# Kernel tuning notes

Hardware: AMD Instinct MI355X
Metric: run time of the kernel (lower is better)

## Reference

```python
import jax, jax.numpy as jnp
import numpy as np

N, E, H, ED, S = 20000, 320000, 256, 64, 4  # nodes, edges, hidden, edge_dim, message_steps


def setup_inputs() -> dict:
    key = jax.random.key(0)
    ks = jax.random.split(key, 20)
    w = lambda k, shape: jax.random.normal(k, shape, dtype=jnp.float32) * 0.02
    inp = {
        "node_state": jax.random.normal(ks[0], (N, H), dtype=jnp.float32),
        "edge_attr": jax.random.normal(ks[1], (E, ED), dtype=jnp.float32),
        # per-step stacked parameters (S steps)
        "nn_g": jnp.ones((S, H), jnp.float32),  # node_norm gamma
        "nn_b": jnp.zeros((S, H), jnp.float32),
        "mn_g": jnp.ones((S, H), jnp.float32),  # msg_norm gamma
        "mn_b": jnp.zeros((S, H), jnp.float32),
        "eW1": w(ks[2], (S, 2 * H + ED, H)), "eb1": jnp.zeros((S, H), jnp.float32),
        "eW2": w(ks[3], (S, H, H)),          "eb2": jnp.zeros((S, H), jnp.float32),
        "nW1": w(ks[4], (S, 2 * H, 2 * H)),  "nb1": jnp.zeros((S, 2 * H), jnp.float32),
        "nW2": w(ks[5], (S, 2 * H, H)),      "nb2": jnp.zeros((S, H), jnp.float32),
        "edge_index": jax.random.randint(ks[6], (2, E), 0, N, dtype=jnp.int64),
    }
    return inp


def _layer_norm(x, g, b, eps=1e-5):
    m = jnp.mean(x, axis=-1, keepdims=True)
    v = jnp.var(x, axis=-1, keepdims=True)
    return (x - m) * jax.lax.rsqrt(v + eps) * g + b


def reference(node_state, edge_attr, nn_g, nn_b, mn_g, mn_b,
              eW1, eb1, eW2, eb2, nW1, nb1, nW2, nb2, edge_index):
    n = node_state.shape[0]
    src, dst = edge_index[0], edge_index[1]
    ones = jnp.ones((dst.shape[0], 1), node_state.dtype)
    deg = jax.ops.segment_sum(ones, dst, num_segments=n)  # [N,1], same each step
    deg = jnp.maximum(deg, 1.0)
    h = node_state
    for i in range(nn_g.shape[0]):  # fixed small number of message steps
        hn = _layer_norm(h, nn_g[i], nn_b[i])                       # [N,H]
        x = jnp.concatenate([hn[src], hn[dst], edge_attr], axis=1)  # [E,2H+ED]
        msg = jax.nn.silu(x @ eW1[i] + eb1[i]) @ eW2[i] + eb2[i]    # [E,H]
        agg = jax.ops.segment_sum(msg, dst, num_segments=n)         # [N,H]
        agg = _layer_norm(agg / deg, mn_g[i], mn_b[i])
        y = jnp.concatenate([hn, agg], axis=1)                      # [N,2H]
        h = h + (jax.nn.silu(y @ nW1[i] + nb1[i]) @ nW2[i] + nb2[i])
    return h
```

## Files before the change

### kernel.cpp

```cpp
#include <hip/hip_runtime.h>
#include <hip/hip_bf16.h>
#include <stdint.h>

#define NN 20000
#define NE 320000
#define HH 256
#define EDK 64
#define NSTEPS 4
#define ECH 80000
#define NCHUNK 4
#define WSTEP 606208

typedef __attribute__((ext_vector_type(8))) short bf16x8;
typedef __attribute__((ext_vector_type(4))) float f32x4;

__device__ __forceinline__ float silu_f(float x) { return x / (1.0f + __expf(-x)); }

__device__ __forceinline__ unsigned short f2bf(float f) {
    __hip_bfloat16 h = __float2bfloat16(f);
    return __builtin_bit_cast(unsigned short, h);
}
__device__ __forceinline__ float bf2f(unsigned short u) {
    unsigned int x = ((unsigned int)u) << 16;
    return __builtin_bit_cast(float, x);
}
__device__ __forceinline__ unsigned int pk2(float a, float b) {
    return (unsigned int)f2bf(a) | ((unsigned int)f2bf(b) << 16);
}

__global__ void ln_kernel(const float* __restrict__ x, const float* __restrict__ g,
                          const float* __restrict__ b, float* __restrict__ y, int M)
{
    int row  = blockIdx.x * 4 + (threadIdx.x >> 6);
    int lane = threadIdx.x & 63;
    if (row >= M) return;
    float4 v = *(const float4*)(x + (size_t)row * HH + lane * 4);
    float s  = v.x + v.y + v.z + v.w;
    float ss = v.x*v.x + v.y*v.y + v.z*v.z + v.w*v.w;
#pragma unroll
    for (int off = 32; off > 0; off >>= 1) {
        s  += __shfl_down(s, off);
        ss += __shfl_down(ss, off);
    }
    float mean = __shfl(s, 0) * (1.0f / HH);
    float ms   = __shfl(ss, 0) * (1.0f / HH);
    float rstd = rsqrtf(ms - mean * mean + 1e-5f);
    float4 gg = *(const float4*)(g + lane * 4);
    float4 bb = *(const float4*)(b + lane * 4);
    float4 o;
    o.x = (v.x - mean) * rstd * gg.x + bb.x;
    o.y = (v.y - mean) * rstd * gg.y + bb.y;
    o.z = (v.z - mean) * rstd * gg.z + bb.z;
    o.w = (v.w - mean) * rstd * gg.w + bb.w;
    *(float4*)(y + (size_t)row * HH + lane * 4) = o;
}

__global__ void wtr_kernel(const float* __restrict__ eW1, const float* __restrict__ eW2,
                           const float* __restrict__ nW1, const float* __restrict__ nW2,
                           unsigned short* __restrict__ wbuf)
{
    int bx = blockIdx.x;
    int s  = bx / 592, t = bx % 592;
    const float* e1 = eW1 + (size_t)s * 576 * 256;
    unsigned short* wb = wbuf + (size_t)s * WSTEP;
    const float* src; unsigned short* dst; int K, N;
    if      (t < 64)  { src = e1;                          K = 256; N = 256; dst = wb; }
    else if (t < 128) { src = e1 + 65536;                  K = 256; N = 256; dst = wb + 65536;  t -= 64; }
    else if (t < 144) { src = e1 + 131072;                 K = 64;  N = 256; dst = wb + 131072; t -= 128; }
    else if (t < 208) { src = eW2 + (size_t)s * 65536;     K = 256; N = 256; dst = wb + 147456; t -= 144; }
    else if (t < 464) { src = nW1 + (size_t)s * 262144;    K = 512; N = 512; dst = wb + 212992; t -= 208; }
    else              { src = nW2 + (size_t)s * 131072;    K = 512; N = 256; dst = wb + 475136; t -= 464; }
    int ntn = N >> 5;
    int tk = t / ntn, tn = t % ntn;
    int k0 = tk * 32, n0 = tn * 32;
    __shared__ float ts[32][33];
    int tx = threadIdx.x & 31, ty = threadIdx.x >> 5;
#pragma unroll
    for (int i = 0; i < 4; i++)
        ts[ty + i * 8][tx] = src[(size_t)(k0 + ty + i * 8) * N + n0 + tx];
    __syncthreads();
#pragma unroll
    for (int i = 0; i < 4; i++)
        dst[(size_t)(n0 + ty + i * 8) * K + k0 + tx] = f2bf(ts[tx][ty + i * 8]);
}

__global__ void easort_kernel(const float* __restrict__ ea, const int* __restrict__ eorig,
                              unsigned short* __restrict__ out)
{
    int gid = blockIdx.x * 256 + threadIdx.x;
    int p = gid >> 4, q = gid & 15;
    if (p >= NE) return;
    float4 v = *(const float4*)(ea + (size_t)eorig[p] * EDK + q * 4);
    ushort4 o;
    o.x = f2bf(v.x); o.y = f2bf(v.y); o.z = f2bf(v.z); o.w = f2bf(v.w);
    *(ushort4*)(out + (size_t)p * EDK + q * 4) = o;
}

#define GBM 128
#define GBN 128
#define GBK 64
template <int EPI, int ASRC, bool BF16OUT>
__global__ __launch_bounds__(256) void mgemm(
    const void* __restrict__ A, const float* __restrict__ A2, int lda,
    const unsigned short* __restrict__ BT,
    const float* __restrict__ bias, const int* __restrict__ cnt,
    void* __restrict__ Cout, int M, int Nc, int K)
{
    __shared__ unsigned short smem[GBM * GBK + GBN * GBK];
    unsigned short* lsA = smem;
    unsigned short* lsB = smem + GBM * GBK;
    const int tid = threadIdx.x;
    const int row0 = blockIdx.x * GBM, col0 = blockIdx.y * GBN;
    const int r = tid >> 1, half = tid & 1;
    const int w = tid >> 6, l = tid & 63;
    const int wm = w >> 1, wn = w & 1;

    const float* Af = (const float*)A;
    const unsigned short* Ab = (const unsigned short*)A;
    int grow = row0 + r;
    bool aval = (grow < M);
    const unsigned short* brow = BT + (size_t)(col0 + r) * K;

    f32x4 acc[4][4] = {};

    for (int k0 = 0; k0 < K; k0 += GBK) {
        if constexpr (ASRC == 3) {
            uint4 q[4] = {};
            if (aval) {
                const unsigned short* ap = Ab + (size_t)grow * lda + k0 + half * 32;
#pragma unroll
                for (int ci = 0; ci < 4; ci++) q[ci] = ((const uint4*)ap)[ci];
            }
#pragma unroll
            for (int ci = 0; ci < 4; ci++) {
                int slot = half * 4 + ci;
                int phys = slot ^ (r & 7);
                *(uint4*)&lsA[r * GBK + phys * 8] = q[ci];
            }
        } else {
            const float* ap = nullptr;
            if constexpr (ASRC == 2) {
                if (aval) ap = ((k0 < 256) ? Af : A2) + (size_t)grow * 256 + (k0 & 255) + half * 32;
            } else {
                if (aval) ap = Af + (size_t)grow * lda + k0 + half * 32;
            }
            float4 fv[8];
            if (ap) {
#pragma unroll
                for (int i = 0; i < 8; i++) fv[i] = ((const float4*)ap)[i];
            } else {
#pragma unroll
                for (int i = 0; i < 8; i++) fv[i] = make_float4(0.f, 0.f, 0.f, 0.f);
            }
#pragma unroll
            for (int ci = 0; ci < 4; ci++) {
                uint4 q;
                q.x = pk2(fv[2*ci].x,   fv[2*ci].y);
                q.y = pk2(fv[2*ci].z,   fv[2*ci].w);
                q.z = pk2(fv[2*ci+1].x, fv[2*ci+1].y);
                q.w = pk2(fv[2*ci+1].z, fv[2*ci+1].w);
                int slot = half * 4 + ci;
                int phys = slot ^ (r & 7);
                *(uint4*)&lsA[r * GBK + phys * 8] = q;
            }
        }
        {
            const unsigned short* bp = brow + k0 + half * 32;
#pragma unroll
            for (int ci = 0; ci < 4; ci++) {
                uint4 q = ((const uint4*)bp)[ci];
                int slot = half * 4 + ci;
                int phys = slot ^ (r & 7);
                *(uint4*)&lsB[r * GBK + phys * 8] = q;
            }
        }
        __syncthreads();
#pragma unroll
        for (int ks = 0; ks < 2; ks++) {
            bf16x8 bfr[4];
#pragma unroll
            for (int n = 0; n < 4; n++) {
                int rn = wn * 64 + n * 16 + (l & 15);
                int phys = (ks * 4 + (l >> 4)) ^ (rn & 7);
                bfr[n] = *(bf16x8*)&lsB[rn * GBK + phys * 8];
            }
#pragma unroll
            for (int m = 0; m < 4; m++) {
                int rm = wm * 64 + m * 16 + (l & 15);
                int phys = (ks * 4 + (l >> 4)) ^ (rm & 7);
                bf16x8 af = *(bf16x8*)&lsA[rm * GBK + phys * 8];
#pragma unroll
                for (int n = 0; n < 4; n++)
                    acc[m][n] = __builtin_amdgcn_mfma_f32_16x16x32_bf16(af, bfr[n], acc[m][n], 0, 0, 0);
            }
        }
        __syncthreads();
    }

    if constexpr (BF16OUT) {
        unsigned short* Cb = (unsigned short*)Cout;
#pragma unroll
        for (int n = 0; n < 4; n++) {
            int cl = wn * 64 + n * 16 + (l & 15);
            float bv = bias ? bias[col0 + cl] : 0.0f;
#pragma unroll
            for (int m = 0; m < 4; m++) {
                int rbase = wm * 64 + m * 16 + (l >> 4) * 4;
#pragma unroll
                for (int i = 0; i < 4; i++) {
                    int rl = rbase + i;
                    float o = acc[m][n][i] + bv;
                    if (EPI == 1) o = silu_f(o);
                    int chunk = cl >> 3;
                    int phys = chunk ^ (rl & 15);
                    smem[rl * 128 + phys * 8 + (cl & 7)] = f2bf(o);
                }
            }
        }
        __syncthreads();
        int orow = tid >> 1, hf = tid & 1;
        int rr = row0 + orow;
        if (rr < M) {
            unsigned short* crow = Cb + (size_t)rr * Nc + col0;
#pragma unroll
            for (int c8 = 0; c8 < 8; c8++) {
                int chunk = hf * 8 + c8;
                int phys = chunk ^ (orow & 15);
                uint4 v = *(uint4*)&smem[orow * 128 + phys * 8];
                *(uint4*)(crow + chunk * 8) = v;
            }
        }
    } else {
        float* Cf = (float*)Cout;
        const int cbase = col0 + wn * 64 + (l & 15);
#pragma unroll
        for (int n = 0; n < 4; n++) {
            int c = cbase + n * 16;
            float bv = bias ? bias[c] : 0.0f;
#pragma unroll
            for (int m = 0; m < 4; m++) {
                int rbase = row0 + wm * 64 + m * 16 + (l >> 4) * 4;
#pragma unroll
                for (int i = 0; i < 4; i++) {
                    int rr = rbase + i;
                    if (rr >= M) continue;
                    float o = acc[m][n][i];
                    if (EPI == 2) {
                        float cf = (float)cnt[rr];
                        o = (o + cf * bv) / fmaxf(cf, 1.0f);
                    } else {
                        o += bv;
                        if (EPI == 1) o = silu_f(o);
                    }
                    size_t off = (size_t)rr * Nc + c;
                    if (EPI == 3) Cf[off] += o;
                    else          Cf[off] = o;
                }
            }
        }
    }
}

__global__ void agg_kernel(const unsigned short* __restrict__ Pab,
                           const unsigned short* __restrict__ Pe, const int* __restrict__ esrc,
                           const int* __restrict__ rowptr,
                           float* __restrict__ u, int e0, int e1)
{
    int node = blockIdx.x * 4 + (threadIdx.x >> 6);
    if (node >= NN) return;
    int beg = rowptr[node], end = rowptr[node + 1];
    int lo = beg > e0 ? beg : e0;
    int hi = end < e1 ? end : e1;
    if (lo >= hi) return;
    int lane = threadIdx.x & 63;
    int j = lane * 4;
    ushort4 pb4 = *(const ushort4*)(Pab + (size_t)node * 512 + 256 + j);
    float b0 = bf2f(pb4.x), b1 = bf2f(pb4.y), b2 = bf2f(pb4.z), b3 = bf2f(pb4.w);
    float a0 = 0.f, a1 = 0.f, a2 = 0.f, a3 = 0.f;
    int src_n = esrc[lo];
    for (int p = lo; p < hi; ++p) {
        int src = src_n;
        if (p + 1 < hi) src_n = esrc[p + 1];
        ushort4 pa4 = *(const ushort4*)(Pab + (size_t)src * 512 + j);
        ushort4 pe4 = *(const ushort4*)(Pe + (size_t)(p - e0) * HH + j);
        a0 += silu_f(bf2f(pa4.x) + b0 + bf2f(pe4.x));
        a1 += silu_f(bf2f(pa4.y) + b1 + bf2f(pe4.y));
        a2 += silu_f(bf2f(pa4.z) + b2 + bf2f(pe4.z));
        a3 += silu_f(bf2f(pa4.w) + b3 + bf2f(pe4.w));
    }
    float* up = u + (size_t)node * HH + j;
    float4 uo = *(const float4*)up;
    uo.x += a0; uo.y += a1; uo.z += a2; uo.w += a3;
    *(float4*)up = uo;
}

__global__ void detect_kernel(const uint32_t* __restrict__ w, int* flag)
{
    int i = blockIdx.x * 256 + threadIdx.x;
    bool bad = false;
    if (i < NE) {
        uint32_t lo = w[2 * i], hi = w[2 * i + 1];
        bad = (hi != 0u) || (lo >= (uint32_t)NN);
    }
    if (__any(bad)) {
        if ((threadIdx.x & 63) == 0) atomicAnd(flag, 0);
    }
}
__global__ void convert_kernel(const uint32_t* __restrict__ w, const int* __restrict__ flag,
                               int* __restrict__ out)
{
    int i = blockIdx.x * 256 + threadIdx.x;
    if (i >= 2 * NE) return;
    out[i] = (*flag) ? (int)w[2 * i] : (int)w[i];
}
__global__ void deg_kernel(const int* __restrict__ idx, int* __restrict__ cnt)
{
    int e = blockIdx.x * 256 + threadIdx.x;
    if (e < NE) atomicAdd(cnt + idx[NE + e], 1);
}

__global__ void scan_kernel(const int* __restrict__ cnt, int* __restrict__ rowptr)
{
    __shared__ int part[1024];
    const int T = 1024, PER = (NN + T - 1) / T;
    int t = threadIdx.x;
    int base = t * PER;
    int s = 0;
    for (int i = 0; i < PER; i++) {
        int idx = base + i;
        if (idx < NN) s += cnt[idx];
    }
    part[t] = s;
    __syncthreads();
    for (int off = 1; off < T; off <<= 1) {
        int v = (t >= off) ? part[t - off] : 0;
        __syncthreads();
        part[t] += v;
        __syncthreads();
    }
    int run = (t == 0) ? 0 : part[t - 1];
    for (int i = 0; i < PER; i++) {
        int idx = base + i;
        if (idx < NN) { rowptr[idx] = run; run += cnt[idx]; }
    }
    if (t == T - 1) rowptr[NN] = part[T - 1];
}

__global__ void fill_kernel(const int* __restrict__ idx, const int* __restrict__ rowptr,
                            int* __restrict__ fillc, int* __restrict__ esrc,
                            int* __restrict__ eorig)
{
    int e = blockIdx.x * 256 + threadIdx.x;
    if (e >= NE) return;
    int dst = idx[NE + e];
    int pos = rowptr[dst] + atomicAdd(fillc + dst, 1);
    esrc[pos]  = idx[e];
    eorig[pos] = e;
}

extern "C" void kernel_launch(void* const* d_in, const int* in_sizes, int n_in,
                              void* d_out, int out_size, void* d_ws, size_t ws_size,
                              hipStream_t stream)
{
    const float* node_state = (const float*)d_in[0];
    const float* edge_attr  = (const float*)d_in[1];
    const float* nn_g = (const float*)d_in[2];
    const float* nn_b = (const float*)d_in[3];
    const float* mn_g = (const float*)d_in[4];
    const float* mn_b = (const float*)d_in[5];
    const float* eW1  = (const float*)d_in[6];
    const float* eb1  = (const float*)d_in[7];
    const float* eW2  = (const float*)d_in[8];
    const float* eb2  = (const float*)d_in[9];
    const float* nW1  = (const float*)d_in[10];
    const float* nb1  = (const float*)d_in[11];
    const float* nW2  = (const float*)d_in[12];
    const float* nb2  = (const float*)d_in[13];
    const uint32_t* eidx_raw = (const uint32_t*)d_in[14];

    const size_t SZ = (size_t)NN * HH;
    float* hn = (float*)d_ws;
    float* u  = hn + SZ;
    unsigned short* Pab = (unsigned short*)(u + SZ);
    unsigned short* eas = Pab + (size_t)NN * 512;
    unsigned short* Pe  = eas + (size_t)NE * EDK;
    float* aggb = (float*)Pe;
    unsigned short* zb = (unsigned short*)((char*)Pe + (size_t)NN * HH * 4);
    unsigned short* wbuf = Pe + (size_t)ECH * HH;
    int* idx32  = (int*)(wbuf + 4 * WSTEP);
    int* esrc   = idx32 + 2 * NE;
    int* eorig  = esrc + NE;
    int* rowptr = eorig + NE;
    int* cnt    = rowptr + NN + 1;
    int* fillc  = cnt + NN;
    int* flag   = fillc + NN;
    size_t needed = ((size_t)(flag + 1) - (size_t)d_ws);
    if (ws_size < needed) return;

    float* h = (float*)d_out;

    hipMemcpyAsync(h, node_state, SZ * sizeof(float), hipMemcpyDeviceToDevice, stream);

    wtr_kernel<<<4 * 592, 256, 0, stream>>>(eW1, eW2, nW1, nW2, wbuf);
    hipMemsetAsync(flag, 0xFF, sizeof(int), stream);
    detect_kernel<<<(NE + 255) / 256, 256, 0, stream>>>(eidx_raw, flag);
    convert_kernel<<<(2 * NE + 255) / 256, 256, 0, stream>>>(eidx_raw, flag, idx32);
    hipMemsetAsync(cnt, 0, NN * sizeof(int), stream);
    deg_kernel<<<(NE + 255) / 256, 256, 0, stream>>>(idx32, cnt);
    scan_kernel<<<1, 1024, 0, stream>>>(cnt, rowptr);
    hipMemsetAsync(fillc, 0, NN * sizeof(int), stream);
    fill_kernel<<<(NE + 255) / 256, 256, 0, stream>>>(idx32, rowptr, fillc, esrc, eorig);
    easort_kernel<<<(NE * 16) / 256, 256, 0, stream>>>(edge_attr, eorig, eas);

    const dim3 gN2((NN + GBM - 1) / GBM, 2);
    const dim3 gN4((NN + GBM - 1) / GBM, 4);
    const dim3 gPe(ECH / GBM, 2);

    for (int s = 0; s < NSTEPS; s++) {
        const unsigned short* wb = wbuf + (size_t)s * WSTEP;
        const unsigned short* WabT = wb;
        const unsigned short* WcT  = wb + 131072;
        const unsigned short* eW2T = wb + 147456;
        const unsigned short* nW1T = wb + 212992;
        const unsigned short* nW2T = wb + 475136;
        const float* eb1s = eb1 + (size_t)s * HH;
        const float* eb2s = eb2 + (size_t)s * HH;
        const float* nb1s = nb1 + (size_t)s * 512;
        const float* nb2s = nb2 + (size_t)s * HH;

        ln_kernel<<<NN / 4, 256, 0, stream>>>(h, nn_g + s * HH, nn_b + s * HH, hn, NN);
        mgemm<0, 0, true><<<gN4, 256, 0, stream>>>(hn, nullptr, HH, WabT, nullptr, nullptr, Pab, NN, 512, HH);
        hipMemsetAsync(u, 0, SZ * sizeof(float), stream);
        for (int c = 0; c < NCHUNK; c++) {
            int e0 = c * ECH, e1 = e0 + ECH;
            mgemm<0, 3, true><<<gPe, 256, 0, stream>>>(eas + (size_t)e0 * EDK, nullptr, EDK, WcT, eb1s, nullptr, Pe, ECH, HH, EDK);
            agg_kernel<<<(NN + 3) / 4, 256, 0, stream>>>(Pab, Pe, esrc, rowptr, u, e0, e1);
        }
        mgemm<2, 0, false><<<gN2, 256, 0, stream>>>(u, nullptr, HH, eW2T, eb2s, cnt, aggb, NN, HH, HH);
        ln_kernel<<<NN / 4, 256, 0, stream>>>(aggb, mn_g + s * HH, mn_b + s * HH, aggb, NN);
        mgemm<1, 2, true><<<gN4, 256, 0, stream>>>(hn, aggb, HH, nW1T, nb1s, nullptr, zb, NN, 512, 512);
        mgemm<3, 3, false><<<gN2, 256, 0, stream>>>(zb, nullptr, 512, nW2T, nb2s, nullptr, h, NN, HH, 512);
    }
}
```

Before: 1.855 ms.

## Store intermediates in bf16, halve edge chunks, and prefetch in aggregation

LayerNorm outputs, the aggregation buffer and the message-norm output are now stored as bf16 rather than fp32. GEMMs read them directly as bf16 with no in-kernel conversion, which cuts memory traffic. Edge processing uses two chunks of 160000 instead of four. The first aggregation pass overwrites the buffer, so the memset is gone, and the gather loop is software-pipelined one edge ahead. The trade-off is accumulating partial sums in bf16 across chunks, which loses precision, and a larger Pe workspace that relies on hard-coded buffer offsets.

```diff
diff --git a/kernel.cpp b/kernel.cpp
--- a/kernel.cpp
+++ b/kernel.cpp
@@ -7,8 +7,8 @@
 #define HH 256
 #define EDK 64
 #define NSTEPS 4
-#define ECH 80000
-#define NCHUNK 4
+#define ECH 160000
+#define NCHUNK 2
 #define WSTEP 606208
 
 typedef __attribute__((ext_vector_type(8))) short bf16x8;
@@ -29,7 +29,7 @@
 }
 
 __global__ void ln_kernel(const float* __restrict__ x, const float* __restrict__ g,
-                          const float* __restrict__ b, float* __restrict__ y, int M)
+                          const float* __restrict__ b, unsigned short* __restrict__ y, int M)
 {
     int row  = blockIdx.x * 4 + (threadIdx.x >> 6);
     int lane = threadIdx.x & 63;
@@ -47,12 +47,12 @@
     float rstd = rsqrtf(ms - mean * mean + 1e-5f);
     float4 gg = *(const float4*)(g + lane * 4);
     float4 bb = *(const float4*)(b + lane * 4);
-    float4 o;
-    o.x = (v.x - mean) * rstd * gg.x + bb.x;
-    o.y = (v.y - mean) * rstd * gg.y + bb.y;
-    o.z = (v.z - mean) * rstd * gg.z + bb.z;
-    o.w = (v.w - mean) * rstd * gg.w + bb.w;
-    *(float4*)(y + (size_t)row * HH + lane * 4) = o;
+    ushort4 o;
+    o.x = f2bf((v.x - mean) * rstd * gg.x + bb.x);
+    o.y = f2bf((v.y - mean) * rstd * gg.y + bb.y);
+    o.z = f2bf((v.z - mean) * rstd * gg.z + bb.z);
+    o.w = f2bf((v.w - mean) * rstd * gg.w + bb.w);
+    *(ushort4*)(y + (size_t)row * HH + lane * 4) = o;
 }
 
 __global__ void wtr_kernel(const float* __restrict__ eW1, const float* __restrict__ eW2,
@@ -101,7 +101,7 @@
 #define GBK 64
 template <int EPI, int ASRC, bool BF16OUT>
 __global__ __launch_bounds__(256) void mgemm(
-    const void* __restrict__ A, const float* __restrict__ A2, int lda,
+    const void* __restrict__ A, const void* __restrict__ A2, int lda,
     const unsigned short* __restrict__ BT,
     const float* __restrict__ bias, const int* __restrict__ cnt,
     void* __restrict__ Cout, int M, int Nc, int K)
@@ -117,6 +117,7 @@
 
     const float* Af = (const float*)A;
     const unsigned short* Ab = (const unsigned short*)A;
+    const unsigned short* A2b = (const unsigned short*)A2;
     int grow = row0 + r;
     bool aval = (grow < M);
     const unsigned short* brow = BT + (size_t)(col0 + r) * K;
@@ -124,10 +125,14 @@
     f32x4 acc[4][4] = {};
 
     for (int k0 = 0; k0 < K; k0 += GBK) {
-        if constexpr (ASRC == 3) {
+        if constexpr (ASRC == 3 || ASRC == 4) {
             uint4 q[4] = {};
             if (aval) {
-                const unsigned short* ap = Ab + (size_t)grow * lda + k0 + half * 32;
+                const unsigned short* ap;
+                if constexpr (ASRC == 4)
+                    ap = ((k0 < 256) ? Ab : A2b) + (size_t)grow * 256 + (k0 & 255) + half * 32;
+                else
+                    ap = Ab + (size_t)grow * lda + k0 + half * 32;
 #pragma unroll
                 for (int ci = 0; ci < 4; ci++) q[ci] = ((const uint4*)ap)[ci];
             }
@@ -138,14 +143,9 @@
                 *(uint4*)&lsA[r * GBK + phys * 8] = q[ci];
             }
         } else {
-            const float* ap = nullptr;
-            if constexpr (ASRC == 2) {
-                if (aval) ap = ((k0 < 256) ? Af : A2) + (size_t)grow * 256 + (k0 & 255) + half * 32;
-            } else {
-                if (aval) ap = Af + (size_t)grow * lda + k0 + half * 32;
-            }
             float4 fv[8];
-            if (ap) {
+            if (aval) {
+                const float* ap = Af + (size_t)grow * lda + k0 + half * 32;
 #pragma unroll
                 for (int i = 0; i < 8; i++) fv[i] = ((const float4*)ap)[i];
             } else {
@@ -261,37 +261,52 @@
     }
 }
 
+template <bool FIRST>
 __global__ void agg_kernel(const unsigned short* __restrict__ Pab,
                            const unsigned short* __restrict__ Pe, const int* __restrict__ esrc,
                            const int* __restrict__ rowptr,
-                           float* __restrict__ u, int e0, int e1)
+                           unsigned short* __restrict__ u, int e0, int e1)
 {
     int node = blockIdx.x * 4 + (threadIdx.x >> 6);
     if (node >= NN) return;
     int beg = rowptr[node], end = rowptr[node + 1];
     int lo = beg > e0 ? beg : e0;
     int hi = end < e1 ? end : e1;
-    if (lo >= hi) return;
+    if (!FIRST && lo >= hi) return;
     int lane = threadIdx.x & 63;
     int j = lane * 4;
-    ushort4 pb4 = *(const ushort4*)(Pab + (size_t)node * 512 + 256 + j);
-    float b0 = bf2f(pb4.x), b1 = bf2f(pb4.y), b2 = bf2f(pb4.z), b3 = bf2f(pb4.w);
     float a0 = 0.f, a1 = 0.f, a2 = 0.f, a3 = 0.f;
-    int src_n = esrc[lo];
-    for (int p = lo; p < hi; ++p) {
-        int src = src_n;
-        if (p + 1 < hi) src_n = esrc[p + 1];
-        ushort4 pa4 = *(const ushort4*)(Pab + (size_t)src * 512 + j);
-        ushort4 pe4 = *(const ushort4*)(Pe + (size_t)(p - e0) * HH + j);
-        a0 += silu_f(bf2f(pa4.x) + b0 + bf2f(pe4.x));
-        a1 += silu_f(bf2f(pa4.y) + b1 + bf2f(pe4.y));
-        a2 += silu_f(bf2f(pa4.z) + b2 + bf2f(pe4.z));
-        a3 += silu_f(bf2f(pa4.w) + b3 + bf2f(pe4.w));
-    }
-    float* up = u + (size_t)node * HH + j;
-    float4 uo = *(const float4*)up;
-    uo.x += a0; uo.y += a1; uo.z += a2; uo.w += a3;
-    *(float4*)up = uo;
+    if (lo < hi) {
+        ushort4 pb4 = *(const ushort4*)(Pab + (size_t)node * 512 + 256 + j);
+        float b0 = bf2f(pb4.x), b1 = bf2f(pb4.y), b2 = bf2f(pb4.z), b3 = bf2f(pb4.w);
+        int p = lo;
+        int src = esrc[p];
+        ushort4 pa = *(const ushort4*)(Pab + (size_t)src * 512 + j);
+        ushort4 pe = *(const ushort4*)(Pe + (size_t)(p - e0) * HH + j);
+        for (;;) {
+            ushort4 cpa = pa, cpe = pe;
+            int np = p + 1;
+            if (np < hi) {
+                int s2 = esrc[np];
+                pa = *(const ushort4*)(Pab + (size_t)s2 * 512 + j);
+                pe = *(const ushort4*)(Pe + (size_t)(np - e0) * HH + j);
+            }
+            a0 += silu_f(bf2f(cpa.x) + b0 + bf2f(cpe.x));
+            a1 += silu_f(bf2f(cpa.y) + b1 + bf2f(cpe.y));
+            a2 += silu_f(bf2f(cpa.z) + b2 + bf2f(cpe.z));
+            a3 += silu_f(bf2f(cpa.w) + b3 + bf2f(cpe.w));
+            if (np >= hi) break;
+            p = np;
+        }
+    }
+    unsigned short* up = u + (size_t)node * HH + j;
+    if (!FIRST) {
+        ushort4 uo = *(const ushort4*)up;
+        a0 += bf2f(uo.x); a1 += bf2f(uo.y); a2 += bf2f(uo.z); a3 += bf2f(uo.w);
+    }
+    ushort4 o;
+    o.x = f2bf(a0); o.y = f2bf(a1); o.z = f2bf(a2); o.w = f2bf(a3);
+    *(ushort4*)up = o;
 }
 
 __global__ void detect_kernel(const uint32_t* __restrict__ w, int* flag)
@@ -303,7 +318,7 @@
         bad = (hi != 0u) || (lo >= (uint32_t)NN);
     }
     if (__any(bad)) {
-        if ((threadIdx.x & 63) == 0) atomicAnd(flag, 0);
+        if ((threadIdx.x & 63) == 0) *flag = 0;
     }
 }
 __global__ void convert_kernel(const uint32_t* __restrict__ w, const int* __restrict__ flag,
@@ -379,13 +394,14 @@
     const uint32_t* eidx_raw = (const uint32_t*)d_in[14];
 
     const size_t SZ = (size_t)NN * HH;
-    float* hn = (float*)d_ws;
-    float* u  = hn + SZ;
-    unsigned short* Pab = (unsigned short*)(u + SZ);
+    unsigned short* hn  = (unsigned short*)d_ws;
+    unsigned short* u   = hn + SZ;
+    unsigned short* Pab = u + SZ;
     unsigned short* eas = Pab + (size_t)NN * 512;
     unsigned short* Pe  = eas + (size_t)NE * EDK;
-    float* aggb = (float*)Pe;
-    unsigned short* zb = (unsigned short*)((char*)Pe + (size_t)NN * HH * 4);
+    float* aggp = (float*)Pe;
+    unsigned short* aggb = (unsigned short*)((char*)Pe + 22000000);
+    unsigned short* zb   = (unsigned short*)((char*)Pe + 34000000);
     unsigned short* wbuf = Pe + (size_t)ECH * HH;
     int* idx32  = (int*)(wbuf + 4 * WSTEP);
     int* esrc   = idx32 + 2 * NE;
@@ -429,16 +445,16 @@
         const float* nb2s = nb2 + (size_t)s * HH;
 
         ln_kernel<<<NN / 4, 256, 0, stream>>>(h, nn_g + s * HH, nn_b + s * HH, hn, NN);
-        mgemm<0, 0, true><<<gN4, 256, 0, stream>>>(hn, nullptr, HH, WabT, nullptr, nullptr, Pab, NN, 512, HH);
-        hipMemsetAsync(u, 0, SZ * sizeof(float), stream);
-        for (int c = 0; c < NCHUNK; c++) {
-            int e0 = c * ECH, e1 = e0 + ECH;
-            mgemm<0, 3, true><<<gPe, 256, 0, stream>>>(eas + (size_t)e0 * EDK, nullptr, EDK, WcT, eb1s, nullptr, Pe, ECH, HH, EDK);
-            agg_kernel<<<(NN + 3) / 4, 256, 0, stream>>>(Pab, Pe, esrc, rowptr, u, e0, e1);
-        }
-        mgemm<2, 0, false><<<gN2, 256, 0, stream>>>(u, nullptr, HH, eW2T, eb2s, cnt, aggb, NN, HH, HH);
-        ln_kernel<<<NN / 4, 256, 0, stream>>>(aggb, mn_g + s * HH, mn_b + s * HH, aggb, NN);
-        mgemm<1, 2, true><<<gN4, 256, 0, stream>>>(hn, aggb, HH, nW1T, nb1s, nullptr, zb, NN, 512, 512);
+        mgemm<0, 3, true><<<gN4, 256, 0, stream>>>(hn, nullptr, HH, WabT, nullptr, nullptr, Pab, NN, 512, HH);
+        {
+            mgemm<0, 3, true><<<gPe, 256, 0, stream>>>(eas, nullptr, EDK, WcT, eb1s, nullptr, Pe, ECH, HH, EDK);
+            agg_kernel<true><<<(NN + 3) / 4, 256, 0, stream>>>(Pab, Pe, esrc, rowptr, u, 0, ECH);
+            mgemm<0, 3, true><<<gPe, 256, 0, stream>>>(eas + (size_t)ECH * EDK, nullptr, EDK, WcT, eb1s, nullptr, Pe, ECH, HH, EDK);
+            agg_kernel<false><<<(NN + 3) / 4, 256, 0, stream>>>(Pab, Pe, esrc, rowptr, u, ECH, NE);
+        }
+        mgemm<2, 3, false><<<gN2, 256, 0, stream>>>(u, nullptr, HH, eW2T, eb2s, cnt, aggp, NN, HH, HH);
+        ln_kernel<<<NN / 4, 256, 0, stream>>>(aggp, mn_g + s * HH, mn_b + s * HH, aggb, NN);
+        mgemm<1, 4, true><<<gN4, 256, 0, stream>>>(hn, aggb, HH, nW1T, nb1s, nullptr, zb, NN, 512, 512);
         mgemm<3, 3, false><<<gN2, 256, 0, stream>>>(zb, nullptr, 512, nW2T, nb2s, nullptr, h, NN, HH, 512);
     }
 }
```

Measured after the change: 1.690 ms. 1.1x faster.
